# Kernel tuning notes

Hardware: AMD Instinct MI355X
Metric: run time of the kernel (lower is better)

## Reference

```python
import jax, jax.numpy as jnp
import numpy as np

N = 64        # n_nodes per graph
H = 128       # hidden channels (128x0e + 128x1o)
NB = 8        # radial bessel basis size
L = 2         # num_interactions
R_MAX = 5.0
AVG_NEIGH = 63.0
DIM = 3       # output vector dim
B = 64        # batch (vmapped)
T = 32        # time-embedding dim
S = 5         # num_species


def _edges(n):
    # fully-connected graph, no self loops (static shapes, jit-friendly)
    s, r = np.meshgrid(np.arange(n), np.arange(n), indexing='ij')
    m = s != r
    return jnp.asarray(s[m]), jnp.asarray(r[m])


def setup_inputs() -> dict:
    key = jax.random.key(0)
    ks = jax.random.split(key, 12)
    sc = 0.05
    return {
        'positions': jax.random.normal(ks[0], (B, N, 3), jnp.float32),
        'node_features': jax.random.randint(ks[1], (B, N), 0, S).astype(jnp.int64),
        'global_features': jax.random.normal(ks[2], (B, T), jnp.float32),
        'emb': jax.random.normal(ks[3], (S, H), jnp.float32) * sc,
        'Wt': jax.random.normal(ks[4], (T, H), jnp.float32) * sc,
        'Wr1': jax.random.normal(ks[5], (L, NB, H), jnp.float32) * sc,
        'Wr2': jax.random.normal(ks[6], (L, H, H), jnp.float32) * sc,
        'Wupd': jax.random.normal(ks[7], (L, H, H), jnp.float32) * sc,
        'Wmix': jax.random.normal(ks[8], (L, H, H), jnp.float32) * sc,
        'Wg1': jax.random.normal(ks[9], (H, H), jnp.float32) * sc,
        'Wg2': jax.random.normal(ks[10], (H, H), jnp.float32) * sc,
        'final_scaling': jnp.ones((), jnp.float32),
    }


def _call_single(pos, z, t, emb, Wt, Wr1, Wr2, Wupd, Wmix, Wg1, Wg2, final_scaling):
    snd, rcv = _edges(N)
    ev = pos[rcv] - pos[snd]                               # [E,3] edge vectors (gather)
    r = jnp.sqrt(jnp.sum(ev * ev, axis=-1) + 1e-12)        # [E]
    u = ev / r[:, None]                                    # unit directions
    # Bessel radial basis with cosine cutoff (r_max acts as soft radius graph)
    n = jnp.arange(1, NB + 1, dtype=pos.dtype)
    rb = jnp.sin(n * jnp.pi * r[:, None] / R_MAX) / r[:, None]   # [E,NB]
    fc = 0.5 * (jnp.cos(jnp.pi * r / R_MAX) + 1.0) * (r < R_MAX)
    rb = rb * fc[:, None]
    # node embedding from species + time embedding
    h = emb[z] + t @ Wt                                    # [N,H] scalar features
    v = jnp.zeros((N, H, DIM), pos.dtype)                  # vector (1o) features
    for l in range(L):
        w = jax.nn.silu(rb @ Wr1[l]) @ Wr2[l]              # [E,H] radial weights
        m0 = w * h[snd]                                    # [E,H] scalar messages
        m1 = m0[:, :, None] * u[:, None, :]                # [E,H,3] vector messages
        a0 = jax.ops.segment_sum(m0, rcv, num_segments=N) / AVG_NEIGH
        a1 = jax.ops.segment_sum(m1, rcv, num_segments=N) / AVG_NEIGH
        h = h + a0 @ Wupd[l]
        v = v + jnp.einsum('ngd,gh->nhd', a1, Wmix[l])
    # equivariant readout: scalar gate per channel contracts vector channels
    g = jax.nn.silu(h @ Wg1) @ Wg2                         # [N,H]
    out = jnp.einsum('nhd,nh->nd', v, g)                   # [N,3]
    return out * final_scaling


def reference(positions, node_features, global_features, emb, Wt, Wr1, Wr2, Wupd, Wmix, Wg1, Wg2, final_scaling):
    f = lambda p, z, t: _call_single(p, z, t, emb, Wt, Wr1, Wr2, Wupd, Wmix, Wg1, Wg2, final_scaling)
    return jax.vmap(f)(positions, node_features, global_features)
```

## Files before the change

kernel.cpp:

```cpp
#include <hip/hip_runtime.h>
#include <math.h>

#define NN 64
#define HH 128
#define NBB 8
#define TT 32
#define BB 64
#define NROW (BB * NN)
#define PLANE ((size_t)NROW * HH)
#define WR1OFF (8 * 16384)

typedef __attribute__((ext_vector_type(8))) short short8;
typedef __attribute__((ext_vector_type(4))) float f32x4;
typedef __attribute__((ext_vector_type(2))) float f32x2;

__device__ __forceinline__ float silu_f(float x) {
  return x * __builtin_amdgcn_rcpf(1.0f + __expf(-x));
}

__device__ __forceinline__ unsigned short f2bf(float x) {
  union { float f; unsigned u; } v; v.f = x;
  unsigned r = v.u + 0x7FFFu + ((v.u >> 16) & 1u);
  return (unsigned short)(r >> 16);
}

__device__ __forceinline__ void gemm32(
    const unsigned short (*sA)[136], const unsigned short* __restrict__ Bp,
    int w, int nlo, int quad, f32x4 C[2][2]) {
  short8 bfr[4][2];
#pragma unroll
  for (int kt = 0; kt < 4; ++kt)
#pragma unroll
    for (int nt = 0; nt < 2; ++nt)
      bfr[kt][nt] = *(const short8*)&Bp[((kt * 128 + w * 32 + nt * 16 + nlo) * 4 + quad) * 8];
#pragma unroll
  for (int mt = 0; mt < 2; ++mt) {
    short8 afr[4];
#pragma unroll
    for (int kt = 0; kt < 4; ++kt)
      afr[kt] = *(const short8*)&sA[mt * 16 + nlo][kt * 32 + quad * 8];
#pragma unroll
    for (int nt = 0; nt < 2; ++nt)
#pragma unroll
      for (int kt = 0; kt < 4; ++kt)
        C[mt][nt] = __builtin_amdgcn_mfma_f32_16x16x32_bf16(afr[kt], bfr[kt][nt], C[mt][nt], 0, 0, 0);
  }
}

__global__ __launch_bounds__(256) void k_init(
    const float* __restrict__ emb, const int* __restrict__ z,
    const float* __restrict__ gf, const float* __restrict__ Wt,
    const float* __restrict__ Wr1, const float* __restrict__ Wr2,
    const float* __restrict__ Wupd, const float* __restrict__ Wmix,
    const float* __restrict__ Wg1, const float* __restrict__ Wg2,
    float* __restrict__ h, unsigned short* __restrict__ Wpack) {
  __shared__ float tvec[HH];
  __shared__ int sz[NN];
  int b = blockIdx.x, tid = threadIdx.x;
#pragma unroll
  for (int ii = 0; ii < 8; ++ii) {
    int idx = b * 2048 + ii * 256 + tid;
    int m = idx >> 14;
    int local = idx & 16383;
    float val;
    if (m < 2) val = Wr2[idx];
    else if (m < 4) val = Wupd[idx - 32768];
    else if (m < 6) val = Wmix[idx - 65536];
    else if (m == 6) val = Wg1[local];
    else val = Wg2[local];
    int k = local >> 7, n = local & 127;
    int kt = k >> 5, q = (k >> 3) & 3, j = k & 7;
    Wpack[(idx & ~16383) + (((kt * 128 + n) * 4 + q) * 8) + j] = f2bf(val);
  }
  if (tid < 128) {
    int e = b * 128 + tid;
    int l = e >> 12, p = e & 4095;
    int n = p >> 5, q = (p >> 3) & 3, j = p & 7;
    float val = (q == 0) ? Wr1[l * NBB * HH + j * HH + n] : 0.f;
    Wpack[WR1OFF + l * 4096 + p] = f2bf(val);
  }
  if (tid < NN) sz[tid] = z[b * NN + tid];
  if (tid < HH) {
    float acc = 0.f;
#pragma unroll
    for (int k = 0; k < TT; ++k) acc += gf[b * TT + k] * Wt[k * HH + tid];
    tvec[tid] = acc;
  }
  __syncthreads();
  for (int i = tid; i < NN * HH; i += 256) {
    int n = i >> 7, c = i & 127;
    h[(size_t)b * NN * HH + i] = emb[sz[n] * HH + c] + tvec[c];
  }
}

__global__ __launch_bounds__(256) void k_layer(
    const float* __restrict__ pos,
    const float* __restrict__ hin,
    float* __restrict__ ap,
    const unsigned short* __restrict__ Wpack,
    int l) {
  __shared__ __align__(16) unsigned short sh_S[NN][136];
  __shared__ __align__(16) unsigned short sh_rbh[NN][8];
  __shared__ __align__(16) float sh_u[3][NN];

  int blk = blockIdx.x;
  int b = blk >> 6, r = blk & 63;
  int tid = threadIdx.x;
  int w = tid >> 6, lane = tid & 63;
  int nlo = lane & 15, quad = lane >> 4;

  {
    int s = tid & 63, ksel = tid >> 6;
    const float* pb = pos + b * NN * 3;
    float dx = pb[r * 3 + 0] - pb[s * 3 + 0];
    float dy = pb[r * 3 + 1] - pb[s * 3 + 1];
    float dz = pb[r * 3 + 2] - pb[s * 3 + 2];
    float rr = sqrtf(dx * dx + dy * dy + dz * dz + 1e-12f);
    float inv = __builtin_amdgcn_rcpf(rr);
    if (ksel == 0) {
      sh_u[0][s] = dx * inv; sh_u[1][s] = dy * inv; sh_u[2][s] = dz * inv;
    }
    const float PI_OVER_5 = 0.628318530717958647692f;
    float fc = (s != r && rr < 5.0f) ? 0.5f * (__cosf(PI_OVER_5 * rr) + 1.0f) : 0.0f;
    float base = PI_OVER_5 * rr;
    float sc = inv * fc;
    float r0 = __sinf((float)(ksel * 2 + 1) * base) * sc;
    float r1 = __sinf((float)(ksel * 2 + 2) * base) * sc;
    *(unsigned*)&sh_rbh[s][ksel * 2] = (unsigned)f2bf(r0) | ((unsigned)f2bf(r1) << 16);
  }
  __syncthreads();

  {
    const unsigned short* Wr1p = Wpack + WR1OFF + l * 4096;
    short8 bw[2];
#pragma unroll
    for (int nt = 0; nt < 2; ++nt)
      bw[nt] = *(const short8*)&Wr1p[((w * 32 + nt * 16 + nlo) * 4 + quad) * 8];
    const short8 zero8 = {0, 0, 0, 0, 0, 0, 0, 0};
#pragma unroll
    for (int mtp = 0; mtp < 2; ++mtp) {
      f32x4 Cs[2][2];
#pragma unroll
      for (int mi = 0; mi < 2; ++mi)
#pragma unroll
        for (int nt = 0; nt < 2; ++nt) Cs[mi][nt] = (f32x4){0.f, 0.f, 0.f, 0.f};
#pragma unroll
      for (int mi = 0; mi < 2; ++mi) {
        int mt = mtp * 2 + mi;
        short8 afr = (quad == 0) ? *(const short8*)&sh_rbh[mt * 16 + nlo][0] : zero8;
#pragma unroll
        for (int nt = 0; nt < 2; ++nt)
          Cs[mi][nt] = __builtin_amdgcn_mfma_f32_16x16x32_bf16(afr, bw[nt], Cs[mi][nt], 0, 0, 0);
      }
#pragma unroll
      for (int mi = 0; mi < 2; ++mi)
#pragma unroll
        for (int nt = 0; nt < 2; ++nt)
#pragma unroll
          for (int reg = 0; reg < 4; ++reg) {
            int s = (mtp * 2 + mi) * 16 + quad * 4 + reg;
            int c = w * 32 + nt * 16 + nlo;
            sh_S[s][c] = f2bf(silu_f(Cs[mi][nt][reg]));
          }
    }
  }
  __syncthreads();

  const unsigned short* Bbase = Wpack + l * 16384;
  short8 bfr[4][2];
#pragma unroll
  for (int kt = 0; kt < 4; ++kt)
#pragma unroll
    for (int nt = 0; nt < 2; ++nt) {
      int c = w * 32 + nt * 16 + nlo;
      bfr[kt][nt] = *(const short8*)&Bbase[((kt * 128 + c) * 4 + quad) * 8];
    }
  float acc0[2] = {0.f, 0.f};
  float a1x[2] = {0.f, 0.f};
  float a1y[2] = {0.f, 0.f};
  float a1z[2] = {0.f, 0.f};
  const float* hb = hin + (size_t)b * NN * HH;

#pragma unroll
  for (int mt = 0; mt < 4; ++mt) {
    short8 afr[4];
    int s_a = mt * 16 + nlo;
#pragma unroll
    for (int kt = 0; kt < 4; ++kt)
      afr[kt] = *(const short8*)&sh_S[s_a][kt * 32 + quad * 8];
    float ux[4], uy[4], uz[4];
#pragma unroll
    for (int reg = 0; reg < 4; ++reg) {
      int s = mt * 16 + quad * 4 + reg;
      ux[reg] = sh_u[0][s]; uy[reg] = sh_u[1][s]; uz[reg] = sh_u[2][s];
    }
#pragma unroll
    for (int nt = 0; nt < 2; ++nt) {
      int c = w * 32 + nt * 16 + nlo;
      f32x4 C = {0.f, 0.f, 0.f, 0.f};
#pragma unroll
      for (int kt = 0; kt < 4; ++kt)
        C = __builtin_amdgcn_mfma_f32_16x16x32_bf16(afr[kt], bfr[kt][nt], C, 0, 0, 0);
#pragma unroll
      for (int reg = 0; reg < 4; ++reg) {
        int s = mt * 16 + quad * 4 + reg;
        float m0 = C[reg] * hb[s * HH + c];
        acc0[nt] += m0;
        a1x[nt] += m0 * ux[reg];
        a1y[nt] += m0 * uy[reg];
        a1z[nt] += m0 * uz[reg];
      }
    }
  }

  const float invAvg = 1.0f / 63.0f;
#pragma unroll
  for (int nt = 0; nt < 2; ++nt) {
    float q0 = acc0[nt], q1 = a1x[nt], q2 = a1y[nt], q3 = a1z[nt];
    q0 += __shfl_xor(q0, 16); q0 += __shfl_xor(q0, 32);
    q1 += __shfl_xor(q1, 16); q1 += __shfl_xor(q1, 32);
    q2 += __shfl_xor(q2, 16); q2 += __shfl_xor(q2, 32);
    q3 += __shfl_xor(q3, 16); q3 += __shfl_xor(q3, 32);
    if (quad == 0) {
      size_t base = (size_t)blk * HH + w * 32 + nt * 16 + nlo;
      ap[base]             = q0 * invAvg;
      ap[PLANE + base]     = q1 * invAvg;
      ap[2 * PLANE + base] = q2 * invAvg;
      ap[3 * PLANE + base] = q3 * invAvg;
    }
  }
}

__global__ __launch_bounds__(256) void k_update(
    const float* __restrict__ ap, const float* __restrict__ hin,
    float* __restrict__ hout, float* __restrict__ vp,
    const unsigned short* __restrict__ Wpack) {
  __shared__ __align__(16) unsigned short sh_a[4][32][136];
  int tid = threadIdx.x, w = tid >> 6, lane = tid & 63;
  int nlo = lane & 15, quad = lane >> 4;
  int row0 = blockIdx.x * 32;
#pragma unroll
  for (int p = 0; p < 4; ++p)
    for (int i = tid; i < 32 * 64; i += 256) {
      int rr = i >> 6, c2 = (i & 63) * 2;
      f32x2 t = *(const f32x2*)&ap[p * PLANE + (size_t)(row0 + rr) * HH + c2];
      *(unsigned*)&sh_a[p][rr][c2] = (unsigned)f2bf(t.x) | ((unsigned)f2bf(t.y) << 16);
    }
  __syncthreads();
  f32x4 Ch[2][2], Cx[2][2], Cy[2][2], Cz[2][2];
#pragma unroll
  for (int mt = 0; mt < 2; ++mt)
#pragma unroll
    for (int nt = 0; nt < 2; ++nt) {
      Ch[mt][nt] = (f32x4){0,0,0,0}; Cx[mt][nt] = (f32x4){0,0,0,0};
      Cy[mt][nt] = (f32x4){0,0,0,0}; Cz[mt][nt] = (f32x4){0,0,0,0};
    }
  gemm32(sh_a[0], Wpack + 2 * 16384, w, nlo, quad, Ch);
  gemm32(sh_a[1], Wpack + 4 * 16384, w, nlo, quad, Cx);
  gemm32(sh_a[2], Wpack + 4 * 16384, w, nlo, quad, Cy);
  gemm32(sh_a[3], Wpack + 4 * 16384, w, nlo, quad, Cz);
#pragma unroll
  for (int mt = 0; mt < 2; ++mt)
#pragma unroll
    for (int nt = 0; nt < 2; ++nt)
#pragma unroll
      for (int reg = 0; reg < 4; ++reg) {
        size_t row = row0 + mt * 16 + quad * 4 + reg;
        int col = w * 32 + nt * 16 + nlo;
        hout[row * HH + col] = hin[row * HH + col] + Ch[mt][nt][reg];
        vp[0 * PLANE + row * HH + col] = Cx[mt][nt][reg];
        vp[1 * PLANE + row * HH + col] = Cy[mt][nt][reg];
        vp[2 * PLANE + row * HH + col] = Cz[mt][nt][reg];
      }
}

__global__ __launch_bounds__(256) void k_update_ro(
    const float* __restrict__ ap, const float* __restrict__ hin,
    const float* __restrict__ vp,
    const unsigned short* __restrict__ Wpack,
    const float* __restrict__ fs, float* __restrict__ out) {
  __shared__ __align__(16) unsigned short sh_a[4][32][136];
  __shared__ __align__(16) unsigned short sh_h[32][136];
  __shared__ float red[4][32][3];
  int tid = threadIdx.x, w = tid >> 6, lane = tid & 63;
  int nlo = lane & 15, quad = lane >> 4;
  int row0 = blockIdx.x * 32;
#pragma unroll
  for (int p = 0; p < 4; ++p)
    for (int i = tid; i < 32 * 64; i += 256) {
      int rr = i >> 6, c2 = (i & 63) * 2;
      f32x2 t = *(const f32x2*)&ap[p * PLANE + (size_t)(row0 + rr) * HH + c2];
      *(unsigned*)&sh_a[p][rr][c2] = (unsigned)f2bf(t.x) | ((unsigned)f2bf(t.y) << 16);
    }
  __syncthreads();
  f32x4 Ch[2][2], Cx[2][2], Cy[2][2], Cz[2][2];
#pragma unroll
  for (int mt = 0; mt < 2; ++mt)
#pragma unroll
    for (int nt = 0; nt < 2; ++nt) {
      Ch[mt][nt] = (f32x4){0,0,0,0}; Cx[mt][nt] = (f32x4){0,0,0,0};
      Cy[mt][nt] = (f32x4){0,0,0,0}; Cz[mt][nt] = (f32x4){0,0,0,0};
    }
  gemm32(sh_a[0], Wpack + 3 * 16384, w, nlo, quad, Ch);
  gemm32(sh_a[1], Wpack + 5 * 16384, w, nlo, quad, Cx);
  gemm32(sh_a[2], Wpack + 5 * 16384, w, nlo, quad, Cy);
  gemm32(sh_a[3], Wpack + 5 * 16384, w, nlo, quad, Cz);
#pragma unroll
  for (int mt = 0; mt < 2; ++mt)
#pragma unroll
    for (int nt = 0; nt < 2; ++nt)
#pragma unroll
      for (int reg = 0; reg < 4; ++reg) {
        int rl = mt * 16 + quad * 4 + reg;
        size_t row = row0 + rl;
        int col = w * 32 + nt * 16 + nlo;
        sh_h[rl][col] = f2bf(hin[row * HH + col] + Ch[mt][nt][reg]);
        Cx[mt][nt][reg] += vp[0 * PLANE + row * HH + col];
        Cy[mt][nt][reg] += vp[1 * PLANE + row * HH + col];
        Cz[mt][nt][reg] += vp[2 * PLANE + row * HH + col];
      }
  __syncthreads();
  unsigned short (*sh_q)[136] = sh_a[0];
  f32x4 Cq[2][2];
#pragma unroll
  for (int mt = 0; mt < 2; ++mt)
#pragma unroll
    for (int nt = 0; nt < 2; ++nt) Cq[mt][nt] = (f32x4){0,0,0,0};
  gemm32(sh_h, Wpack + 6 * 16384, w, nlo, quad, Cq);
#pragma unroll
  for (int mt = 0; mt < 2; ++mt)
#pragma unroll
    for (int nt = 0; nt < 2; ++nt)
#pragma unroll
      for (int reg = 0; reg < 4; ++reg)
        sh_q[mt * 16 + quad * 4 + reg][w * 32 + nt * 16 + nlo] = f2bf(silu_f(Cq[mt][nt][reg]));
  __syncthreads();
  f32x4 Cg[2][2];
#pragma unroll
  for (int mt = 0; mt < 2; ++mt)
#pragma unroll
    for (int nt = 0; nt < 2; ++nt) Cg[mt][nt] = (f32x4){0,0,0,0};
  gemm32(sh_q, Wpack + 7 * 16384, w, nlo, quad, Cg);
  float pr[3][2][4];
#pragma unroll
  for (int d = 0; d < 3; ++d)
#pragma unroll
    for (int mt = 0; mt < 2; ++mt)
#pragma unroll
      for (int reg = 0; reg < 4; ++reg) pr[d][mt][reg] = 0.f;
#pragma unroll
  for (int mt = 0; mt < 2; ++mt)
#pragma unroll
    for (int nt = 0; nt < 2; ++nt)
#pragma unroll
      for (int reg = 0; reg < 4; ++reg) {
        float gv = Cg[mt][nt][reg];
        pr[0][mt][reg] += gv * Cx[mt][nt][reg];
        pr[1][mt][reg] += gv * Cy[mt][nt][reg];
        pr[2][mt][reg] += gv * Cz[mt][nt][reg];
      }
#pragma unroll
  for (int off = 1; off < 16; off <<= 1)
#pragma unroll
    for (int d = 0; d < 3; ++d)
#pragma unroll
      for (int mt = 0; mt < 2; ++mt)
#pragma unroll
        for (int reg = 0; reg < 4; ++reg)
          pr[d][mt][reg] += __shfl_xor(pr[d][mt][reg], off);
  if (nlo == 0) {
#pragma unroll
    for (int d = 0; d < 3; ++d)
#pragma unroll
      for (int mt = 0; mt < 2; ++mt)
#pragma unroll
        for (int reg = 0; reg < 4; ++reg)
          red[w][mt * 16 + quad * 4 + reg][d] = pr[d][mt][reg];
  }
  __syncthreads();
  if (tid < 96) {
    int row = tid / 3, d = tid % 3;
    float s = red[0][row][d] + red[1][row][d] + red[2][row][d] + red[3][row][d];
    out[(size_t)(row0 + row) * 3 + d] = s * fs[0];
  }
}

extern "C" void kernel_launch(void* const* d_in, const int* in_sizes, int n_in,
                              void* d_out, int out_size, void* d_ws, size_t ws_size,
                              hipStream_t stream) {
  const float* pos  = (const float*)d_in[0];
  const int*   z    = (const int*)d_in[1];
  const float* gf   = (const float*)d_in[2];
  const float* emb  = (const float*)d_in[3];
  const float* Wt   = (const float*)d_in[4];
  const float* Wr1  = (const float*)d_in[5];
  const float* Wr2  = (const float*)d_in[6];
  const float* Wupd = (const float*)d_in[7];
  const float* Wmix = (const float*)d_in[8];
  const float* Wg1  = (const float*)d_in[9];
  const float* Wg2  = (const float*)d_in[10];
  const float* fs   = (const float*)d_in[11];
  float* out = (float*)d_out;

  float* ws = (float*)d_ws;
  float* hA = ws;
  float* hB = ws + PLANE;
  float* vp = ws + 2 * PLANE;
  float* apl = ws + 5 * PLANE;
  unsigned short* Wpack = (unsigned short*)(ws + 9 * PLANE);

  k_init<<<dim3(BB), dim3(256), 0, stream>>>(emb, z, gf, Wt, Wr1, Wr2, Wupd,
                                             Wmix, Wg1, Wg2, hA, Wpack);
  k_layer<<<dim3(NROW), dim3(256), 0, stream>>>(pos, hA, apl, Wpack, 0);
  k_update<<<dim3(128), dim3(256), 0, stream>>>(apl, hA, hB, vp, Wpack);
  k_layer<<<dim3(NROW), dim3(256), 0, stream>>>(pos, hB, apl, Wpack, 1);
  k_update_ro<<<dim3(128), dim3(256), 0, stream>>>(apl, hB, vp, Wpack, fs, out);
}
```

Measured before the change: 167.2 us.

## Process two receivers per layer block and halve update-kernel row tiles

Measured after the change: 155.6 us. 1.07x faster.

```diff
diff --git a/kernel.cpp b/kernel.cpp
--- a/kernel.cpp
+++ b/kernel.cpp
@@ -24,27 +24,20 @@
   return (unsigned short)(r >> 16);
 }
 
-__device__ __forceinline__ void gemm32(
+__device__ __forceinline__ void gemm16(
     const unsigned short (*sA)[136], const unsigned short* __restrict__ Bp,
-    int w, int nlo, int quad, f32x4 C[2][2]) {
-  short8 bfr[4][2];
+    int w, int nlo, int quad, f32x4 C[2]) {
+  short8 afr[4];
 #pragma unroll
   for (int kt = 0; kt < 4; ++kt)
-#pragma unroll
-    for (int nt = 0; nt < 2; ++nt)
-      bfr[kt][nt] = *(const short8*)&Bp[((kt * 128 + w * 32 + nt * 16 + nlo) * 4 + quad) * 8];
-#pragma unroll
-  for (int mt = 0; mt < 2; ++mt) {
-    short8 afr[4];
-#pragma unroll
-    for (int kt = 0; kt < 4; ++kt)
-      afr[kt] = *(const short8*)&sA[mt * 16 + nlo][kt * 32 + quad * 8];
-#pragma unroll
-    for (int nt = 0; nt < 2; ++nt)
-#pragma unroll
-      for (int kt = 0; kt < 4; ++kt)
-        C[mt][nt] = __builtin_amdgcn_mfma_f32_16x16x32_bf16(afr[kt], bfr[kt][nt], C[mt][nt], 0, 0, 0);
-  }
+    afr[kt] = *(const short8*)&sA[nlo][kt * 32 + quad * 8];
+#pragma unroll
+  for (int nt = 0; nt < 2; ++nt)
+#pragma unroll
+    for (int kt = 0; kt < 4; ++kt) {
+      short8 bfr = *(const short8*)&Bp[((kt * 128 + w * 32 + nt * 16 + nlo) * 4 + quad) * 8];
+      C[nt] = __builtin_amdgcn_mfma_f32_16x16x32_bf16(afr[kt], bfr, C[nt], 0, 0, 0);
+    }
 }
 
 __global__ __launch_bounds__(256) void k_init(
@@ -99,18 +92,32 @@
     float* __restrict__ ap,
     const unsigned short* __restrict__ Wpack,
     int l) {
-  __shared__ __align__(16) unsigned short sh_S[NN][136];
-  __shared__ __align__(16) unsigned short sh_rbh[NN][8];
-  __shared__ __align__(16) float sh_u[3][NN];
+  __shared__ __align__(16) unsigned short sh_S[2][NN][136];
+  __shared__ __align__(16) unsigned short sh_rbh[2][NN][8];
+  __shared__ __align__(16) float sh_u[2][3][NN];
 
   int blk = blockIdx.x;
-  int b = blk >> 6, r = blk & 63;
+  int b = blk >> 5, rp = blk & 31;
+  int r0 = rp * 2;
   int tid = threadIdx.x;
   int w = tid >> 6, lane = tid & 63;
   int nlo = lane & 15, quad = lane >> 4;
+  const float* hb = hin + (size_t)b * NN * HH;
+
+  float hbv[4][2][4];
+#pragma unroll
+  for (int mt = 0; mt < 4; ++mt)
+#pragma unroll
+    for (int nt = 0; nt < 2; ++nt)
+#pragma unroll
+      for (int reg = 0; reg < 4; ++reg)
+        hbv[mt][nt][reg] = hb[(mt * 16 + quad * 4 + reg) * HH + w * 32 + nt * 16 + nlo];
 
   {
-    int s = tid & 63, ksel = tid >> 6;
+    int s = tid & 63;
+    int ksel = (tid >> 6) & 1;
+    int ri = (tid >> 7) & 1;
+    int r = r0 + ri;
     const float* pb = pos + b * NN * 3;
     float dx = pb[r * 3 + 0] - pb[s * 3 + 0];
     float dy = pb[r * 3 + 1] - pb[s * 3 + 1];
@@ -118,15 +125,19 @@
     float rr = sqrtf(dx * dx + dy * dy + dz * dz + 1e-12f);
     float inv = __builtin_amdgcn_rcpf(rr);
     if (ksel == 0) {
-      sh_u[0][s] = dx * inv; sh_u[1][s] = dy * inv; sh_u[2][s] = dz * inv;
+      sh_u[ri][0][s] = dx * inv; sh_u[ri][1][s] = dy * inv; sh_u[ri][2][s] = dz * inv;
     }
     const float PI_OVER_5 = 0.628318530717958647692f;
     float fc = (s != r && rr < 5.0f) ? 0.5f * (__cosf(PI_OVER_5 * rr) + 1.0f) : 0.0f;
     float base = PI_OVER_5 * rr;
     float sc = inv * fc;
-    float r0 = __sinf((float)(ksel * 2 + 1) * base) * sc;
-    float r1 = __sinf((float)(ksel * 2 + 2) * base) * sc;
-    *(unsigned*)&sh_rbh[s][ksel * 2] = (unsigned)f2bf(r0) | ((unsigned)f2bf(r1) << 16);
+    int k0 = ksel * 4;
+    float v0 = __sinf((float)(k0 + 1) * base) * sc;
+    float v1 = __sinf((float)(k0 + 2) * base) * sc;
+    float v2 = __sinf((float)(k0 + 3) * base) * sc;
+    float v3 = __sinf((float)(k0 + 4) * base) * sc;
+    *(unsigned*)&sh_rbh[ri][s][k0]     = (unsigned)f2bf(v0) | ((unsigned)f2bf(v1) << 16);
+    *(unsigned*)&sh_rbh[ri][s][k0 + 2] = (unsigned)f2bf(v2) | ((unsigned)f2bf(v3) << 16);
   }
   __syncthreads();
 
@@ -138,31 +149,33 @@
       bw[nt] = *(const short8*)&Wr1p[((w * 32 + nt * 16 + nlo) * 4 + quad) * 8];
     const short8 zero8 = {0, 0, 0, 0, 0, 0, 0, 0};
 #pragma unroll
-    for (int mtp = 0; mtp < 2; ++mtp) {
-      f32x4 Cs[2][2];
-#pragma unroll
-      for (int mi = 0; mi < 2; ++mi)
-#pragma unroll
-        for (int nt = 0; nt < 2; ++nt) Cs[mi][nt] = (f32x4){0.f, 0.f, 0.f, 0.f};
-#pragma unroll
-      for (int mi = 0; mi < 2; ++mi) {
-        int mt = mtp * 2 + mi;
-        short8 afr = (quad == 0) ? *(const short8*)&sh_rbh[mt * 16 + nlo][0] : zero8;
-#pragma unroll
-        for (int nt = 0; nt < 2; ++nt)
-          Cs[mi][nt] = __builtin_amdgcn_mfma_f32_16x16x32_bf16(afr, bw[nt], Cs[mi][nt], 0, 0, 0);
+    for (int ri = 0; ri < 2; ++ri)
+#pragma unroll
+      for (int mtp = 0; mtp < 2; ++mtp) {
+        f32x4 Cs[2][2];
+#pragma unroll
+        for (int mi = 0; mi < 2; ++mi)
+#pragma unroll
+          for (int nt = 0; nt < 2; ++nt) Cs[mi][nt] = (f32x4){0.f, 0.f, 0.f, 0.f};
+#pragma unroll
+        for (int mi = 0; mi < 2; ++mi) {
+          int mt = mtp * 2 + mi;
+          short8 afr = (quad == 0) ? *(const short8*)&sh_rbh[ri][mt * 16 + nlo][0] : zero8;
+#pragma unroll
+          for (int nt = 0; nt < 2; ++nt)
+            Cs[mi][nt] = __builtin_amdgcn_mfma_f32_16x16x32_bf16(afr, bw[nt], Cs[mi][nt], 0, 0, 0);
+        }
+#pragma unroll
+        for (int mi = 0; mi < 2; ++mi)
+#pragma unroll
+          for (int nt = 0; nt < 2; ++nt)
+#pragma unroll
+            for (int reg = 0; reg < 4; ++reg) {
+              int s = (mtp * 2 + mi) * 16 + quad * 4 + reg;
+              int c = w * 32 + nt * 16 + nlo;
+              sh_S[ri][s][c] = f2bf(silu_f(Cs[mi][nt][reg]));
+            }
       }
-#pragma unroll
-      for (int mi = 0; mi < 2; ++mi)
-#pragma unroll
-        for (int nt = 0; nt < 2; ++nt)
-#pragma unroll
-          for (int reg = 0; reg < 4; ++reg) {
-            int s = (mtp * 2 + mi) * 16 + quad * 4 + reg;
-            int c = w * 32 + nt * 16 + nlo;
-            sh_S[s][c] = f2bf(silu_f(Cs[mi][nt][reg]));
-          }
-    }
   }
   __syncthreads();
 
@@ -171,62 +184,59 @@
 #pragma unroll
   for (int kt = 0; kt < 4; ++kt)
 #pragma unroll
-    for (int nt = 0; nt < 2; ++nt) {
-      int c = w * 32 + nt * 16 + nlo;
-      bfr[kt][nt] = *(const short8*)&Bbase[((kt * 128 + c) * 4 + quad) * 8];
-    }
-  float acc0[2] = {0.f, 0.f};
-  float a1x[2] = {0.f, 0.f};
-  float a1y[2] = {0.f, 0.f};
-  float a1z[2] = {0.f, 0.f};
-  const float* hb = hin + (size_t)b * NN * HH;
-
-#pragma unroll
-  for (int mt = 0; mt < 4; ++mt) {
-    short8 afr[4];
-    int s_a = mt * 16 + nlo;
-#pragma unroll
-    for (int kt = 0; kt < 4; ++kt)
-      afr[kt] = *(const short8*)&sh_S[s_a][kt * 32 + quad * 8];
-    float ux[4], uy[4], uz[4];
-#pragma unroll
-    for (int reg = 0; reg < 4; ++reg) {
-      int s = mt * 16 + quad * 4 + reg;
-      ux[reg] = sh_u[0][s]; uy[reg] = sh_u[1][s]; uz[reg] = sh_u[2][s];
-    }
-#pragma unroll
-    for (int nt = 0; nt < 2; ++nt) {
-      int c = w * 32 + nt * 16 + nlo;
-      f32x4 C = {0.f, 0.f, 0.f, 0.f};
+    for (int nt = 0; nt < 2; ++nt)
+      bfr[kt][nt] = *(const short8*)&Bbase[((kt * 128 + w * 32 + nt * 16 + nlo) * 4 + quad) * 8];
+
+  const float invAvg = 1.0f / 63.0f;
+#pragma unroll
+  for (int ri = 0; ri < 2; ++ri) {
+    float acc0[2] = {0.f, 0.f};
+    float a1x[2] = {0.f, 0.f};
+    float a1y[2] = {0.f, 0.f};
+    float a1z[2] = {0.f, 0.f};
+#pragma unroll
+    for (int mt = 0; mt < 4; ++mt) {
+      short8 afr[4];
+      int s_a = mt * 16 + nlo;
 #pragma unroll
       for (int kt = 0; kt < 4; ++kt)
-        C = __builtin_amdgcn_mfma_f32_16x16x32_bf16(afr[kt], bfr[kt][nt], C, 0, 0, 0);
+        afr[kt] = *(const short8*)&sh_S[ri][s_a][kt * 32 + quad * 8];
+      float ux[4], uy[4], uz[4];
 #pragma unroll
       for (int reg = 0; reg < 4; ++reg) {
         int s = mt * 16 + quad * 4 + reg;
-        float m0 = C[reg] * hb[s * HH + c];
-        acc0[nt] += m0;
-        a1x[nt] += m0 * ux[reg];
-        a1y[nt] += m0 * uy[reg];
-        a1z[nt] += m0 * uz[reg];
+        ux[reg] = sh_u[ri][0][s]; uy[reg] = sh_u[ri][1][s]; uz[reg] = sh_u[ri][2][s];
       }
-    }
-  }
-
-  const float invAvg = 1.0f / 63.0f;
-#pragma unroll
-  for (int nt = 0; nt < 2; ++nt) {
-    float q0 = acc0[nt], q1 = a1x[nt], q2 = a1y[nt], q3 = a1z[nt];
-    q0 += __shfl_xor(q0, 16); q0 += __shfl_xor(q0, 32);
-    q1 += __shfl_xor(q1, 16); q1 += __shfl_xor(q1, 32);
-    q2 += __shfl_xor(q2, 16); q2 += __shfl_xor(q2, 32);
-    q3 += __shfl_xor(q3, 16); q3 += __shfl_xor(q3, 32);
-    if (quad == 0) {
-      size_t base = (size_t)blk * HH + w * 32 + nt * 16 + nlo;
-      ap[base]             = q0 * invAvg;
-      ap[PLANE + base]     = q1 * invAvg;
-      ap[2 * PLANE + base] = q2 * invAvg;
-      ap[3 * PLANE + base] = q3 * invAvg;
+#pragma unroll
+      for (int nt = 0; nt < 2; ++nt) {
+        f32x4 C = {0.f, 0.f, 0.f, 0.f};
+#pragma unroll
+        for (int kt = 0; kt < 4; ++kt)
+          C = __builtin_amdgcn_mfma_f32_16x16x32_bf16(afr[kt], bfr[kt][nt], C, 0, 0, 0);
+#pragma unroll
+        for (int reg = 0; reg < 4; ++reg) {
+          float m0 = C[reg] * hbv[mt][nt][reg];
+          acc0[nt] += m0;
+          a1x[nt] += m0 * ux[reg];
+          a1y[nt] += m0 * uy[reg];
+          a1z[nt] += m0 * uz[reg];
+        }
+      }
+    }
+#pragma unroll
+    for (int nt = 0; nt < 2; ++nt) {
+      float q0 = acc0[nt], q1 = a1x[nt], q2 = a1y[nt], q3 = a1z[nt];
+      q0 += __shfl_xor(q0, 16); q0 += __shfl_xor(q0, 32);
+      q1 += __shfl_xor(q1, 16); q1 += __shfl_xor(q1, 32);
+      q2 += __shfl_xor(q2, 16); q2 += __shfl_xor(q2, 32);
+      q3 += __shfl_xor(q3, 16); q3 += __shfl_xor(q3, 32);
+      if (quad == 0) {
+        size_t base = (size_t)(b * NN + r0 + ri) * HH + w * 32 + nt * 16 + nlo;
+        ap[base]             = q0 * invAvg;
+        ap[PLANE + base]     = q1 * invAvg;
+        ap[2 * PLANE + base] = q2 * invAvg;
+        ap[3 * PLANE + base] = q3 * invAvg;
+      }
     }
   }
 }
@@ -235,43 +245,37 @@
     const float* __restrict__ ap, const float* __restrict__ hin,
     float* __restrict__ hout, float* __restrict__ vp,
     const unsigned short* __restrict__ Wpack) {
-  __shared__ __align__(16) unsigned short sh_a[4][32][136];
+  __shared__ __align__(16) unsigned short sh_a[4][16][136];
   int tid = threadIdx.x, w = tid >> 6, lane = tid & 63;
   int nlo = lane & 15, quad = lane >> 4;
-  int row0 = blockIdx.x * 32;
+  int row0 = blockIdx.x * 16;
 #pragma unroll
   for (int p = 0; p < 4; ++p)
-    for (int i = tid; i < 32 * 64; i += 256) {
+#pragma unroll
+    for (int ii = 0; ii < 4; ++ii) {
+      int i = ii * 256 + tid;
       int rr = i >> 6, c2 = (i & 63) * 2;
       f32x2 t = *(const f32x2*)&ap[p * PLANE + (size_t)(row0 + rr) * HH + c2];
       *(unsigned*)&sh_a[p][rr][c2] = (unsigned)f2bf(t.x) | ((unsigned)f2bf(t.y) << 16);
     }
   __syncthreads();
-  f32x4 Ch[2][2], Cx[2][2], Cy[2][2], Cz[2][2];
-#pragma unroll
-  for (int mt = 0; mt < 2; ++mt)
-#pragma unroll
-    for (int nt = 0; nt < 2; ++nt) {
-      Ch[mt][nt] = (f32x4){0,0,0,0}; Cx[mt][nt] = (f32x4){0,0,0,0};
-      Cy[mt][nt] = (f32x4){0,0,0,0}; Cz[mt][nt] = (f32x4){0,0,0,0};
-    }
-  gemm32(sh_a[0], Wpack + 2 * 16384, w, nlo, quad, Ch);
-  gemm32(sh_a[1], Wpack + 4 * 16384, w, nlo, quad, Cx);
-  gemm32(sh_a[2], Wpack + 4 * 16384, w, nlo, quad, Cy);
-  gemm32(sh_a[3], Wpack + 4 * 16384, w, nlo, quad, Cz);
-#pragma unroll
-  for (int mt = 0; mt < 2; ++mt)
-#pragma unroll
-    for (int nt = 0; nt < 2; ++nt)
-#pragma unroll
-      for (int reg = 0; reg < 4; ++reg) {
-        size_t row = row0 + mt * 16 + quad * 4 + reg;
-        int col = w * 32 + nt * 16 + nlo;
-        hout[row * HH + col] = hin[row * HH + col] + Ch[mt][nt][reg];
-        vp[0 * PLANE + row * HH + col] = Cx[mt][nt][reg];
-        vp[1 * PLANE + row * HH + col] = Cy[mt][nt][reg];
-        vp[2 * PLANE + row * HH + col] = Cz[mt][nt][reg];
-      }
+  f32x4 Ch[2] = {{0,0,0,0},{0,0,0,0}}, Cx[2] = {{0,0,0,0},{0,0,0,0}};
+  f32x4 Cy[2] = {{0,0,0,0},{0,0,0,0}}, Cz[2] = {{0,0,0,0},{0,0,0,0}};
+  gemm16(sh_a[0], Wpack + 2 * 16384, w, nlo, quad, Ch);
+  gemm16(sh_a[1], Wpack + 4 * 16384, w, nlo, quad, Cx);
+  gemm16(sh_a[2], Wpack + 4 * 16384, w, nlo, quad, Cy);
+  gemm16(sh_a[3], Wpack + 4 * 16384, w, nlo, quad, Cz);
+#pragma unroll
+  for (int nt = 0; nt < 2; ++nt)
+#pragma unroll
+    for (int reg = 0; reg < 4; ++reg) {
+      size_t row = row0 + quad * 4 + reg;
+      int col = w * 32 + nt * 16 + nlo;
+      hout[row * HH + col] = hin[row * HH + col] + Ch[nt][reg];
+      vp[0 * PLANE + row * HH + col] = Cx[nt][reg];
+      vp[1 * PLANE + row * HH + col] = Cy[nt][reg];
+      vp[2 * PLANE + row * HH + col] = Cz[nt][reg];
+    }
 }
 
 __global__ __launch_bounds__(256) void k_update_ro(
@@ -279,106 +283,82 @@
     const float* __restrict__ vp,
     const unsigned short* __restrict__ Wpack,
     const float* __restrict__ fs, float* __restrict__ out) {
-  __shared__ __align__(16) unsigned short sh_a[4][32][136];
-  __shared__ __align__(16) unsigned short sh_h[32][136];
-  __shared__ float red[4][32][3];
+  __shared__ __align__(16) unsigned short sh_a[4][16][136];
+  __shared__ __align__(16) unsigned short sh_h[16][136];
+  __shared__ float red[4][16][3];
   int tid = threadIdx.x, w = tid >> 6, lane = tid & 63;
   int nlo = lane & 15, quad = lane >> 4;
-  int row0 = blockIdx.x * 32;
+  int row0 = blockIdx.x * 16;
 #pragma unroll
   for (int p = 0; p < 4; ++p)
-    for (int i = tid; i < 32 * 64; i += 256) {
+#pragma unroll
+    for (int ii = 0; ii < 4; ++ii) {
+      int i = ii * 256 + tid;
       int rr = i >> 6, c2 = (i & 63) * 2;
       f32x2 t = *(const f32x2*)&ap[p * PLANE + (size_t)(row0 + rr) * HH + c2];
       *(unsigned*)&sh_a[p][rr][c2] = (unsigned)f2bf(t.x) | ((unsigned)f2bf(t.y) << 16);
     }
   __syncthreads();
-  f32x4 Ch[2][2], Cx[2][2], Cy[2][2], Cz[2][2];
-#pragma unroll
-  for (int mt = 0; mt < 2; ++mt)
-#pragma unroll
-    for (int nt = 0; nt < 2; ++nt) {
-      Ch[mt][nt] = (f32x4){0,0,0,0}; Cx[mt][nt] = (f32x4){0,0,0,0};
-      Cy[mt][nt] = (f32x4){0,0,0,0}; Cz[mt][nt] = (f32x4){0,0,0,0};
-    }
-  gemm32(sh_a[0], Wpack + 3 * 16384, w, nlo, quad, Ch);
-  gemm32(sh_a[1], Wpack + 5 * 16384, w, nlo, quad, Cx);
-  gemm32(sh_a[2], Wpack + 5 * 16384, w, nlo, quad, Cy);
-  gemm32(sh_a[3], Wpack + 5 * 16384, w, nlo, quad, Cz);
-#pragma unroll
-  for (int mt = 0; mt < 2; ++mt)
-#pragma unroll
-    for (int nt = 0; nt < 2; ++nt)
-#pragma unroll
-      for (int reg = 0; reg < 4; ++reg) {
-        int rl = mt * 16 + quad * 4 + reg;
-        size_t row = row0 + rl;
-        int col = w * 32 + nt * 16 + nlo;
-        sh_h[rl][col] = f2bf(hin[row * HH + col] + Ch[mt][nt][reg]);
-        Cx[mt][nt][reg] += vp[0 * PLANE + row * HH + col];
-        Cy[mt][nt][reg] += vp[1 * PLANE + row * HH + col];
-        Cz[mt][nt][reg] += vp[2 * PLANE + row * HH + col];
-      }
+  f32x4 Ch[2] = {{0,0,0,0},{0,0,0,0}}, Cx[2] = {{0,0,0,0},{0,0,0,0}};
+  f32x4 Cy[2] = {{0,0,0,0},{0,0,0,0}}, Cz[2] = {{0,0,0,0},{0,0,0,0}};
+  gemm16(sh_a[0], Wpack + 3 * 16384, w, nlo, quad, Ch);
+  gemm16(sh_a[1], Wpack + 5 * 16384, w, nlo, quad, Cx);
+  gemm16(sh_a[2], Wpack + 5 * 16384, w, nlo, quad, Cy);
+  gemm16(sh_a[3], Wpack + 5 * 16384, w, nlo, quad, Cz);
+#pragma unroll
+  for (int nt = 0; nt < 2; ++nt)
+#pragma unroll
+    for (int reg = 0; reg < 4; ++reg) {
+      int rl = quad * 4 + reg;
+      size_t row = row0 + rl;
+      int col = w * 32 + nt * 16 + nlo;
+      sh_h[rl][col] = f2bf(hin[row * HH + col] + Ch[nt][reg]);
+      Cx[nt][reg] += vp[0 * PLANE + row * HH + col];
+      Cy[nt][reg] += vp[1 * PLANE + row * HH + col];
+      Cz[nt][reg] += vp[2 * PLANE + row * HH + col];
+    }
   __syncthreads();
   unsigned short (*sh_q)[136] = sh_a[0];
-  f32x4 Cq[2][2];
-#pragma unroll
-  for (int mt = 0; mt < 2; ++mt)
-#pragma unroll
-    for (int nt = 0; nt < 2; ++nt) Cq[mt][nt] = (f32x4){0,0,0,0};
-  gemm32(sh_h, Wpack + 6 * 16384, w, nlo, quad, Cq);
-#pragma unroll
-  for (int mt = 0; mt < 2; ++mt)
-#pragma unroll
-    for (int nt = 0; nt < 2; ++nt)
+  f32x4 Cq[2] = {{0,0,0,0},{0,0,0,0}};
+  gemm16(sh_h, Wpack + 6 * 16384, w, nlo, quad, Cq);
+#pragma unroll
+  for (int nt = 0; nt < 2; ++nt)
+#pragma unroll
+    for (int reg = 0; reg < 4; ++reg)
+      sh_q[quad * 4 + reg][w * 32 + nt * 16 + nlo] = f2bf(silu_f(Cq[nt][reg]));
+  __syncthreads();
+  f32x4 Cg[2] = {{0,0,0,0},{0,0,0,0}};
+  gemm16(sh_q, Wpack + 7 * 16384, w, nlo, quad, Cg);
+  float pr[3][4];
+#pragma unroll
+  for (int d = 0; d < 3; ++d)
+#pragma unroll
+    for (int reg = 0; reg < 4; ++reg) pr[d][reg] = 0.f;
+#pragma unroll
+  for (int nt = 0; nt < 2; ++nt)
+#pragma unroll
+    for (int reg = 0; reg < 4; ++reg) {
+      float gv = Cg[nt][reg];
+      pr[0][reg] += gv * Cx[nt][reg];
+      pr[1][reg] += gv * Cy[nt][reg];
+      pr[2][reg] += gv * Cz[nt][reg];
+    }
+#pragma unroll
+  for (int off = 1; off < 16; off <<= 1)
+#pragma unroll
+    for (int d = 0; d < 3; ++d)
 #pragma unroll
       for (int reg = 0; reg < 4; ++reg)
-        sh_q[mt * 16 + quad * 4 + reg][w * 32 + nt * 16 + nlo] = f2bf(silu_f(Cq[mt][nt][reg]));
-  __syncthreads();
-  f32x4 Cg[2][2];
-#pragma unroll
-  for (int mt = 0; mt < 2; ++mt)
-#pragma unroll
-    for (int nt = 0; nt < 2; ++nt) Cg[mt][nt] = (f32x4){0,0,0,0};
-  gemm32(sh_q, Wpack + 7 * 16384, w, nlo, quad, Cg);
-  float pr[3][2][4];
-#pragma unroll
-  for (int d = 0; d < 3; ++d)
-#pragma unroll
-    for (int mt = 0; mt < 2; ++mt)
-#pragma unroll
-      for (int reg = 0; reg < 4; ++reg) pr[d][mt][reg] = 0.f;
-#pragma unroll
-  for (int mt = 0; mt < 2; ++mt)
-#pragma unroll
-    for (int nt = 0; nt < 2; ++nt)
-#pragma unroll
-      for (int reg = 0; reg < 4; ++reg) {
-        float gv = Cg[mt][nt][reg];
-        pr[0][mt][reg] += gv * Cx[mt][nt][reg];
-        pr[1][mt][reg] += gv * Cy[mt][nt][reg];
-        pr[2][mt][reg] += gv * Cz[mt][nt][reg];
-      }
-#pragma unroll
-  for (int off = 1; off < 16; off <<= 1)
+        pr[d][reg] += __shfl_xor(pr[d][reg], off);
+  if (nlo == 0) {
 #pragma unroll
     for (int d = 0; d < 3; ++d)
 #pragma unroll
-      for (int mt = 0; mt < 2; ++mt)
-#pragma unroll
-        for (int reg = 0; reg < 4; ++reg)
-          pr[d][mt][reg] += __shfl_xor(pr[d][mt][reg], off);
-  if (nlo == 0) {
-#pragma unroll
-    for (int d = 0; d < 3; ++d)
-#pragma unroll
-      for (int mt = 0; mt < 2; ++mt)
-#pragma unroll
-        for (int reg = 0; reg < 4; ++reg)
-          red[w][mt * 16 + quad * 4 + reg][d] = pr[d][mt][reg];
-  }
-  __syncthreads();
-  if (tid < 96) {
+      for (int reg = 0; reg < 4; ++reg)
+        red[w][quad * 4 + reg][d] = pr[d][reg];
+  }
+  __syncthreads();
+  if (tid < 48) {
     int row = tid / 3, d = tid % 3;
     float s = red[0][row][d] + red[1][row][d] + red[2][row][d] + red[3][row][d];
     out[(size_t)(row0 + row) * 3 + d] = s * fs[0];
@@ -411,8 +391,8 @@
 
   k_init<<<dim3(BB), dim3(256), 0, stream>>>(emb, z, gf, Wt, Wr1, Wr2, Wupd,
                                              Wmix, Wg1, Wg2, hA, Wpack);
-  k_layer<<<dim3(NROW), dim3(256), 0, stream>>>(pos, hA, apl, Wpack, 0);
-  k_update<<<dim3(128), dim3(256), 0, stream>>>(apl, hA, hB, vp, Wpack);
-  k_layer<<<dim3(NROW), dim3(256), 0, stream>>>(pos, hB, apl, Wpack, 1);
-  k_update_ro<<<dim3(128), dim3(256), 0, stream>>>(apl, hB, vp, Wpack, fs, out);
-}
+  k_layer<<<dim3(BB * 32), dim3(256), 0, stream>>>(pos, hA, apl, Wpack, 0);
+  k_update<<<dim3(256), dim3(256), 0, stream>>>(apl, hA, hB, vp, Wpack);
+  k_layer<<<dim3(BB * 32), dim3(256), 0, stream>>>(pos, hB, apl, Wpack, 1);
+  k_update_ro<<<dim3(256), dim3(256), 0, stream>>>(apl, hB, vp, Wpack, fs, out);
+}
```
